# Kernel tuning notes

Hardware: AMD Instinct MI355X
Metric: run time of the kernel (lower is better)

Reference implementation:

```python
import jax, jax.numpy as jnp
import numpy as np

EPS = 1e-12  # torch F.normalize default eps

def _l2norm(x, axis=-1):
    n = jnp.linalg.norm(x, axis=axis, keepdims=True)
    return x / jnp.maximum(n, EPS)

def setup_inputs() -> dict:
    key = jax.random.key(0)
    k1, k2 = jax.random.split(key)
    query = jax.random.normal(k1, (65536, 512), dtype=jnp.float32)
    prototypes = jax.random.normal(k2, (64, 512), dtype=jnp.float32)
    return {"query": query, "prototypes": prototypes, "k": 3}

def reference(query, prototypes, k):
    # cosine similarity between queries and prototypes: [B, P]
    sim = jnp.einsum('bd,pd->bp', _l2norm(query), _l2norm(prototypes))
    k = min(int(k), prototypes.shape[0])
    weights, indices = jax.lax.top_k(sim, k)          # [B, k]
    retrieved = prototypes[indices]                   # [B, k, D]
    w = jax.nn.softmax(weights, axis=1)               # [B, k]
    return jnp.einsum('bkd,bk->bd', retrieved, w)     # [B, D]
```

## Files before the change

### kernel.cpp

```cpp
#include <hip/hip_runtime.h>
#include <math.h>

#define DIM   512
#define NP    64
#define TRB   128
#define BK    32
#define NCH   16
#define ASTR  132
#define TAU   1e-5f
#define RFB   128

#define WS_PTRAW 0
#define WS_INV64 131072
#define WS_INVPF 131584
#define WS_CNT   131840
#define WS_LIST  131968

__device__ __forceinline__ void ins4f(float v, int idx, float& v0, float& v1,
                                      float& v2, float& v3, int& j0, int& j1,
                                      int& j2, int& j3) {
  const bool b0 = v > v0, b1 = v > v1, b2 = v > v2, b3 = v > v3;
  v3 = b2 ? v2 : (b3 ? v : v3);  j3 = b2 ? j2 : (b3 ? idx : j3);
  v2 = b1 ? v1 : (b2 ? v : v2);  j2 = b1 ? j1 : (b2 ? idx : j2);
  v1 = b0 ? v0 : (b1 ? v : v1);  j1 = b0 ? j0 : (b1 ? idx : j1);
  v0 = b0 ? v  : v0;             j0 = b0 ? idx : j0;
}

__device__ __forceinline__ void ins3d(double v, int idx, double& b0, double& b1,
                                      double& b2, int& k0, int& k1, int& k2) {
  const bool c0 = v > b0, c1 = v > b1, c2 = v > b2;
  b2 = c1 ? b1 : (c2 ? v : b2);  k2 = c1 ? k1 : (c2 ? idx : k2);
  b1 = c0 ? b0 : (c1 ? v : b1);  k1 = c0 ? k0 : (c1 ? idx : k1);
  b0 = c0 ? v  : b0;             k0 = c0 ? idx : k0;
}

__global__ __launch_bounds__(256) void prep_kernel(
    const float* __restrict__ protos, float* __restrict__ ptw,
    double* __restrict__ inv64, float* __restrict__ invpf,
    int* __restrict__ cnt) {
  if (blockIdx.x == 0 && threadIdx.x == 0) *cnt = 0;
  const int p = (blockIdx.x * 256 + threadIdx.x) >> 6;
  const int lane = threadIdx.x & 63;
  if (p >= NP) return;
  const float4* pr = (const float4*)(protos + (size_t)p * DIM);
  const float4 a = pr[lane * 2];
  const float4 b = pr[lane * 2 + 1];
  double ss = (double)a.x * a.x + (double)a.y * a.y + (double)a.z * a.z +
              (double)a.w * a.w + (double)b.x * b.x + (double)b.y * b.y +
              (double)b.z * b.z + (double)b.w * b.w;
#pragma unroll
  for (int m = 1; m < 64; m <<= 1) ss += __shfl_xor(ss, m);
  const double inv = 1.0 / fmax(sqrt(ss), 1e-12);
  if (lane == 0) { inv64[p] = inv; invpf[p] = (float)inv; }
  const float v[8] = {a.x, a.y, a.z, a.w, b.x, b.y, b.z, b.w};
#pragma unroll
  for (int e = 0; e < 8; ++e)
    ptw[(size_t)(lane * 8 + e) * NP + p] = v[e];
}

__global__ __launch_bounds__(256, 4) void sim_kernel(
    const float* __restrict__ query, const float* __restrict__ protos,
    const float* __restrict__ ptw, const float* __restrict__ invpf,
    float* __restrict__ out, int* __restrict__ cnt, int* __restrict__ list) {
  __shared__ float Ast[BK * ASTR];
  __shared__ float Bst[BK * NP];
  __shared__ float nredL[TRB * 8];
  __shared__ float qiS[TRB];
  __shared__ float4 wiS[TRB];

  const int t = threadIdx.x;
  const int row0 = blockIdx.x * TRB;
  const int tr = t >> 4;
  const int tp = t & 15;
  const int arow = t >> 3;
  const int acp = t & 7;

  const float* aptr[4];
#pragma unroll
  for (int s = 0; s < 4; ++s)
    aptr[s] = query + (size_t)(row0 + arow + 32 * s) * DIM + acp * 4;
  const float* bptr = ptw + t * 8;

  float acc[8][4] = {};
  float na[4] = {0.f, 0.f, 0.f, 0.f};

  float4 Ar[4], Br0, Br1;
#pragma unroll
  for (int s = 0; s < 4; ++s) Ar[s] = *(const float4*)(aptr[s]);
  Br0 = *(const float4*)(bptr);
  Br1 = *(const float4*)(bptr + 4);

  for (int c = 0; c < NCH; ++c) {
    __syncthreads();
#pragma unroll
    for (int s = 0; s < 4; ++s) {
      const float v[4] = {Ar[s].x, Ar[s].y, Ar[s].z, Ar[s].w};
      const int rl = arow + 32 * s;
#pragma unroll
      for (int e = 0; e < 4; ++e) Ast[(acp * 4 + e) * ASTR + rl] = v[e];
      na[s] += v[0] * v[0] + v[1] * v[1] + v[2] * v[2] + v[3] * v[3];
    }
    *(float4*)&Bst[t * 8] = Br0;
    *(float4*)&Bst[t * 8 + 4] = Br1;
    __syncthreads();
    if (c + 1 < NCH) {
#pragma unroll
      for (int s = 0; s < 4; ++s)
        Ar[s] = *(const float4*)(aptr[s] + (c + 1) * BK);
      Br0 = *(const float4*)(bptr + (c + 1) * BK * NP);
      Br1 = *(const float4*)(bptr + (c + 1) * BK * NP + 4);
    }
#pragma unroll 8
    for (int kk = 0; kk < BK; ++kk) {
      const float4 a0 = *(const float4*)&Ast[kk * ASTR + tr * 8];
      const float4 a1 = *(const float4*)&Ast[kk * ASTR + tr * 8 + 4];
      const float4 b0 = *(const float4*)&Bst[kk * NP + tp * 4];
      const float av[8] = {a0.x, a0.y, a0.z, a0.w, a1.x, a1.y, a1.z, a1.w};
      const float bv[4] = {b0.x, b0.y, b0.z, b0.w};
#pragma unroll
      for (int i = 0; i < 8; ++i)
#pragma unroll
        for (int j = 0; j < 4; ++j)
          acc[i][j] = fmaf(av[i], bv[j], acc[i][j]);
    }
  }

#pragma unroll
  for (int s = 0; s < 4; ++s) nredL[(arow + 32 * s) * 8 + acp] = na[s];
  __syncthreads();
  if (t < TRB) {
    float ssum = 0.f;
#pragma unroll
    for (int e = 0; e < 8; ++e) ssum += nredL[t * 8 + e];
    qiS[t] = 1.0f / fmaxf(sqrtf(ssum), 1e-12f);
  }
  __syncthreads();

  const float4 ipv = *(const float4*)(invpf + tp * 4);
  const float ip[4] = {ipv.x, ipv.y, ipv.z, ipv.w};
#pragma unroll
  for (int i = 0; i < 8; ++i) {
    const int row = tr * 8 + i;
    float v0 = -1e30f, v1 = -1e30f, v2 = -1e30f, v3 = -1e30f;
    int j0 = 0, j1 = 0, j2 = 0, j3 = 0;
#pragma unroll
    for (int j = 0; j < 4; ++j)
      ins4f(acc[i][j] * ip[j], tp * 4 + j, v0, v1, v2, v3, j0, j1, j2, j3);
#pragma unroll
    for (int m = 1; m <= 8; m <<= 1) {
      const float p0 = __shfl_xor(v0, m), p1 = __shfl_xor(v1, m);
      const float p2 = __shfl_xor(v2, m), p3 = __shfl_xor(v3, m);
      const int q0 = __shfl_xor(j0, m), q1 = __shfl_xor(j1, m);
      const int q2 = __shfl_xor(j2, m), q3 = __shfl_xor(j3, m);
      ins4f(p0, q0, v0, v1, v2, v3, j0, j1, j2, j3);
      ins4f(p1, q1, v0, v1, v2, v3, j0, j1, j2, j3);
      ins4f(p2, q2, v0, v1, v2, v3, j0, j1, j2, j3);
      ins4f(p3, q3, v0, v1, v2, v3, j0, j1, j2, j3);
    }
    if (tp == 0) {
      const float qi = qiS[row];
      const float s0 = v0 * qi, s1 = v1 * qi, s2 = v2 * qi, s3 = v3 * qi;
      const float e1 = expf(s1 - s0), e2 = expf(s2 - s0);
      const float inv = 1.0f / (1.0f + e1 + e2);
      wiS[row] = make_float4(inv, e1 * inv, e2 * inv,
                             __int_as_float(j0 | (j1 << 6) | (j2 << 12)));
      if (s2 - s3 < TAU) {
        const int pos = atomicAdd(cnt, 1);
        list[pos] = row0 + row;
      }
    }
  }
  __syncthreads();

  const int wid = t >> 6;
  const int lane = t & 63;
#pragma unroll 4
  for (int it = 0; it < 64; ++it) {
    const int idx = it * 4 + wid;
    const int r = idx >> 1, h = idx & 1;
    const float4 wi = wiS[r];
    const int pack = __float_as_int(wi.w);
    const int i0 = pack & 63, i1 = (pack >> 6) & 63, i2 = (pack >> 12) & 63;
    const float4 pa = ((const float4*)(protos + (size_t)i0 * DIM + h * 256))[lane];
    const float4 pb = ((const float4*)(protos + (size_t)i1 * DIM + h * 256))[lane];
    const float4 pc = ((const float4*)(protos + (size_t)i2 * DIM + h * 256))[lane];
    float4 res;
    res.x = wi.x * pa.x + wi.y * pb.x + wi.z * pc.x;
    res.y = wi.x * pa.y + wi.y * pb.y + wi.z * pc.y;
    res.z = wi.x * pa.z + wi.y * pb.z + wi.z * pc.z;
    res.w = wi.x * pa.w + wi.y * pb.w + wi.z * pc.w;
    ((float4*)(out + (size_t)(row0 + r) * DIM + h * 256))[lane] = res;
  }
}

__global__ __launch_bounds__(256) void refine_kernel(
    const float* __restrict__ query, const float* __restrict__ protos,
    const float* __restrict__ ptw, const double* __restrict__ inv64,
    const int* __restrict__ cnt, const int* __restrict__ list,
    float* __restrict__ out) {
  const int n = *cnt;
  const int lane = threadIdx.x & 63;
  const int gw = blockIdx.x * 4 + (threadIdx.x >> 6);

  for (int i = gw; i < n; i += RFB * 4) {
    const int row = list[i];
    const float* q = query + (size_t)row * DIM;
    double a0 = 0.0, a1 = 0.0, a2 = 0.0, a3 = 0.0;
    float qs = 0.f;
#pragma unroll 4
    for (int k = 0; k < DIM; k += 4) {
      const float4 qv = *(const float4*)(q + k);
      a0 = fma((double)qv.x, (double)ptw[(size_t)(k + 0) * NP + lane], a0);
      a1 = fma((double)qv.y, (double)ptw[(size_t)(k + 1) * NP + lane], a1);
      a2 = fma((double)qv.z, (double)ptw[(size_t)(k + 2) * NP + lane], a2);
      a3 = fma((double)qv.w, (double)ptw[(size_t)(k + 3) * NP + lane], a3);
      qs += qv.x * qv.x + qv.y * qv.y + qv.z * qv.z + qv.w * qv.w;
    }
    const double sim = (a0 + a1 + a2 + a3) * inv64[lane];

    double b0 = sim, b1 = -1e300, b2 = -1e300;
    int k0 = lane, k1 = 0, k2 = 0;
#pragma unroll
    for (int m = 1; m <= 32; m <<= 1) {
      const double p0 = __shfl_xor(b0, m), p1 = __shfl_xor(b1, m),
                   p2 = __shfl_xor(b2, m);
      const int q0 = __shfl_xor(k0, m), q1 = __shfl_xor(k1, m),
                q2 = __shfl_xor(k2, m);
      ins3d(p0, q0, b0, b1, b2, k0, k1, k2);
      ins3d(p1, q1, b0, b1, b2, k0, k1, k2);
      ins3d(p2, q2, b0, b1, b2, k0, k1, k2);
    }
    const double qi = 1.0 / fmax(sqrt((double)qs), 1e-12);
    const double s0 = b0 * qi, s1 = b1 * qi, s2 = b2 * qi;
    const double e1 = exp(s1 - s0), e2 = exp(s2 - s0);
    const double inv = 1.0 / (1.0 + e1 + e2);
    const double w0 = inv, w1 = e1 * inv, w2 = e2 * inv;
    const float* p0r = protos + (size_t)k0 * DIM;
    const float* p1r = protos + (size_t)k1 * DIM;
    const float* p2r = protos + (size_t)k2 * DIM;
#pragma unroll
    for (int u = 0; u < 2; ++u) {
      const int col = u * 256 + lane * 4;
      const float4 x = *(const float4*)(p0r + col);
      const float4 y = *(const float4*)(p1r + col);
      const float4 z = *(const float4*)(p2r + col);
      float4 res;
      res.x = (float)(w0 * x.x + w1 * y.x + w2 * z.x);
      res.y = (float)(w0 * x.y + w1 * y.y + w2 * z.y);
      res.z = (float)(w0 * x.z + w1 * y.z + w2 * z.z);
      res.w = (float)(w0 * x.w + w1 * y.w + w2 * z.w);
      *(float4*)(out + (size_t)row * DIM + col) = res;
    }
  }
}

extern "C" void kernel_launch(void* const* d_in, const int* in_sizes, int n_in,
                              void* d_out, int out_size, void* d_ws, size_t ws_size,
                              hipStream_t stream) {
  const float* query = (const float*)d_in[0];
  const float* protos = (const float*)d_in[1];
  float* out = (float*)d_out;
  float* ptw = (float*)((char*)d_ws + WS_PTRAW);
  double* inv64 = (double*)((char*)d_ws + WS_INV64);
  float* invpf = (float*)((char*)d_ws + WS_INVPF);
  int* cnt = (int*)((char*)d_ws + WS_CNT);
  int* list = (int*)((char*)d_ws + WS_LIST);

  const int nrows = in_sizes[0] / DIM;

  hipLaunchKernelGGL(prep_kernel, dim3(16), dim3(256), 0, stream,
                     protos, ptw, inv64, invpf, cnt);
  hipLaunchKernelGGL(sim_kernel, dim3(nrows / TRB), dim3(256), 0, stream,
                     query, protos, ptw, invpf, out, cnt, list);
  hipLaunchKernelGGL(refine_kernel, dim3(RFB), dim3(256), 0, stream,
                     query, protos, ptw, inv64, cnt, list, out);
}
```

Before: 133.1 us.

## Halve row tile, double-buffer shared tiles with XOR swizzle, shuffle-reduce norms

```diff
diff --git a/kernel.cpp b/kernel.cpp
--- a/kernel.cpp
+++ b/kernel.cpp
@@ -3,10 +3,9 @@
 
 #define DIM   512
 #define NP    64
-#define TRB   128
+#define TRB   64
 #define BK    32
 #define NCH   16
-#define ASTR  132
 #define TAU   1e-5f
 #define RFB   128
 
@@ -62,9 +61,8 @@
     const float* __restrict__ query, const float* __restrict__ protos,
     const float* __restrict__ ptw, const float* __restrict__ invpf,
     float* __restrict__ out, int* __restrict__ cnt, int* __restrict__ list) {
-  __shared__ float Ast[BK * ASTR];
-  __shared__ float Bst[BK * NP];
-  __shared__ float nredL[TRB * 8];
+  __shared__ float Ast[2][BK][64];
+  __shared__ float Bst[2][BK][NP];
   __shared__ float qiS[TRB];
   __shared__ float4 wiS[TRB];
 
@@ -72,75 +70,77 @@
   const int row0 = blockIdx.x * TRB;
   const int tr = t >> 4;
   const int tp = t & 15;
-  const int arow = t >> 3;
-  const int acp = t & 7;
-
-  const float* aptr[4];
-#pragma unroll
-  for (int s = 0; s < 4; ++s)
-    aptr[s] = query + (size_t)(row0 + arow + 32 * s) * DIM + acp * 4;
-  const float* bptr = ptw + t * 8;
-
-  float acc[8][4] = {};
-  float na[4] = {0.f, 0.f, 0.f, 0.f};
-
-  float4 Ar[4], Br0, Br1;
-#pragma unroll
-  for (int s = 0; s < 4; ++s) Ar[s] = *(const float4*)(aptr[s]);
-  Br0 = *(const float4*)(bptr);
-  Br1 = *(const float4*)(bptr + 4);
-
-  for (int c = 0; c < NCH; ++c) {
+  const int sr = t >> 3;
+  const int sc = t & 7;
+  const int bk = t >> 4;
+  const int bp = t & 15;
+
+  const float* aptr0 = query + (size_t)(row0 + sr) * DIM + sc * 4;
+  const float* aptr1 = query + (size_t)(row0 + sr + 32) * DIM + sc * 4;
+  const float* bptr0 = ptw + (size_t)bk * NP + bp * 4;
+  const float* bptr1 = ptw + (size_t)(bk + 16) * NP + bp * 4;
+
+  float acc[4][4] = {};
+  float na0 = 0.f, na1 = 0.f;
+
+  float4 ar0 = *(const float4*)aptr0;
+  float4 ar1 = *(const float4*)aptr1;
+  float4 br0 = *(const float4*)bptr0;
+  float4 br1 = *(const float4*)bptr1;
+
+  const int rsw0 = sr ^ (sc << 2);
+  const int rsw1 = (sr + 32) ^ (sc << 2);
+
+  for (int ch = 0; ch < NCH; ++ch) {
+    const int b = ch & 1;
+    Ast[b][sc * 4 + 0][rsw0] = ar0.x;
+    Ast[b][sc * 4 + 1][rsw0] = ar0.y;
+    Ast[b][sc * 4 + 2][rsw0] = ar0.z;
+    Ast[b][sc * 4 + 3][rsw0] = ar0.w;
+    Ast[b][sc * 4 + 0][rsw1] = ar1.x;
+    Ast[b][sc * 4 + 1][rsw1] = ar1.y;
+    Ast[b][sc * 4 + 2][rsw1] = ar1.z;
+    Ast[b][sc * 4 + 3][rsw1] = ar1.w;
+    *(float4*)&Bst[b][bk][bp * 4] = br0;
+    *(float4*)&Bst[b][bk + 16][bp * 4] = br1;
+    na0 += ar0.x * ar0.x + ar0.y * ar0.y + ar0.z * ar0.z + ar0.w * ar0.w;
+    na1 += ar1.x * ar1.x + ar1.y * ar1.y + ar1.z * ar1.z + ar1.w * ar1.w;
     __syncthreads();
-#pragma unroll
-    for (int s = 0; s < 4; ++s) {
-      const float v[4] = {Ar[s].x, Ar[s].y, Ar[s].z, Ar[s].w};
-      const int rl = arow + 32 * s;
-#pragma unroll
-      for (int e = 0; e < 4; ++e) Ast[(acp * 4 + e) * ASTR + rl] = v[e];
-      na[s] += v[0] * v[0] + v[1] * v[1] + v[2] * v[2] + v[3] * v[3];
-    }
-    *(float4*)&Bst[t * 8] = Br0;
-    *(float4*)&Bst[t * 8 + 4] = Br1;
-    __syncthreads();
-    if (c + 1 < NCH) {
-#pragma unroll
-      for (int s = 0; s < 4; ++s)
-        Ar[s] = *(const float4*)(aptr[s] + (c + 1) * BK);
-      Br0 = *(const float4*)(bptr + (c + 1) * BK * NP);
-      Br1 = *(const float4*)(bptr + (c + 1) * BK * NP + 4);
+    if (ch + 1 < NCH) {
+      ar0 = *(const float4*)(aptr0 + (ch + 1) * BK);
+      ar1 = *(const float4*)(aptr1 + (ch + 1) * BK);
+      br0 = *(const float4*)(bptr0 + (size_t)(ch + 1) * BK * NP);
+      br1 = *(const float4*)(bptr1 + (size_t)(ch + 1) * BK * NP);
     }
 #pragma unroll 8
     for (int kk = 0; kk < BK; ++kk) {
-      const float4 a0 = *(const float4*)&Ast[kk * ASTR + tr * 8];
-      const float4 a1 = *(const float4*)&Ast[kk * ASTR + tr * 8 + 4];
-      const float4 b0 = *(const float4*)&Bst[kk * NP + tp * 4];
-      const float av[8] = {a0.x, a0.y, a0.z, a0.w, a1.x, a1.y, a1.z, a1.w};
-      const float bv[4] = {b0.x, b0.y, b0.z, b0.w};
-#pragma unroll
-      for (int i = 0; i < 8; ++i)
+      const int swz = (kk >> 2) << 2;
+      const float4 a4 = *(const float4*)&Ast[b][kk][(tr * 4) ^ swz];
+      const float4 b4 = *(const float4*)&Bst[b][kk][tp * 4];
+      const float av[4] = {a4.x, a4.y, a4.z, a4.w};
+      const float bv[4] = {b4.x, b4.y, b4.z, b4.w};
+#pragma unroll
+      for (int i = 0; i < 4; ++i)
 #pragma unroll
         for (int j = 0; j < 4; ++j)
           acc[i][j] = fmaf(av[i], bv[j], acc[i][j]);
     }
   }
 
-#pragma unroll
-  for (int s = 0; s < 4; ++s) nredL[(arow + 32 * s) * 8 + acp] = na[s];
-  __syncthreads();
-  if (t < TRB) {
-    float ssum = 0.f;
-#pragma unroll
-    for (int e = 0; e < 8; ++e) ssum += nredL[t * 8 + e];
-    qiS[t] = 1.0f / fmaxf(sqrtf(ssum), 1e-12f);
+  na0 += __shfl_xor(na0, 1); na1 += __shfl_xor(na1, 1);
+  na0 += __shfl_xor(na0, 2); na1 += __shfl_xor(na1, 2);
+  na0 += __shfl_xor(na0, 4); na1 += __shfl_xor(na1, 4);
+  if ((t & 7) == 0) {
+    qiS[sr] = 1.0f / fmaxf(sqrtf(na0), 1e-12f);
+    qiS[sr + 32] = 1.0f / fmaxf(sqrtf(na1), 1e-12f);
   }
   __syncthreads();
 
   const float4 ipv = *(const float4*)(invpf + tp * 4);
   const float ip[4] = {ipv.x, ipv.y, ipv.z, ipv.w};
 #pragma unroll
-  for (int i = 0; i < 8; ++i) {
-    const int row = tr * 8 + i;
+  for (int i = 0; i < 4; ++i) {
+    const int row = tr * 4 + i;
     float v0 = -1e30f, v1 = -1e30f, v2 = -1e30f, v3 = -1e30f;
     int j0 = 0, j1 = 0, j2 = 0, j3 = 0;
 #pragma unroll
@@ -175,7 +175,7 @@
   const int wid = t >> 6;
   const int lane = t & 63;
 #pragma unroll 4
-  for (int it = 0; it < 64; ++it) {
+  for (int it = 0; it < 32; ++it) {
     const int idx = it * 4 + wid;
     const int r = idx >> 1, h = idx & 1;
     const float4 wi = wiS[r];
```

Result: slower. 136.0 us (+2.2%).

## Restructure sim kernel to single-wavefront blocks with double-buffered 8x8 register tiles

Applied to the files above, without the earlier changes.

```diff
diff --git a/kernel.cpp b/kernel.cpp
--- a/kernel.cpp
+++ b/kernel.cpp
@@ -1,20 +1,17 @@
 #include <hip/hip_runtime.h>
 #include <math.h>
 
-#define DIM   512
-#define NP    64
-#define TRB   128
-#define BK    32
-#define NCH   16
-#define ASTR  132
-#define TAU   1e-5f
-#define RFB   128
+#define DIM 512
+#define NP  64
+#define TAU 1e-5f
+#define LISTCAP 8192
+#define RFB 128
 
 #define WS_PTRAW 0
-#define WS_INV64 131072
-#define WS_INVPF 131584
-#define WS_CNT   131840
-#define WS_LIST  131968
+#define WS_PTN   131072
+#define WS_INV64 262144
+#define WS_CNT   262656
+#define WS_LIST  262784
 
 __device__ __forceinline__ void ins4f(float v, int idx, float& v0, float& v1,
                                       float& v2, float& v3, int& j0, int& j1,
@@ -36,7 +33,7 @@
 
 __global__ __launch_bounds__(256) void prep_kernel(
     const float* __restrict__ protos, float* __restrict__ ptw,
-    double* __restrict__ inv64, float* __restrict__ invpf,
+    float* __restrict__ ptn, double* __restrict__ inv64,
     int* __restrict__ cnt) {
   if (blockIdx.x == 0 && threadIdx.x == 0) *cnt = 0;
   const int p = (blockIdx.x * 256 + threadIdx.x) >> 6;
@@ -51,103 +48,109 @@
 #pragma unroll
   for (int m = 1; m < 64; m <<= 1) ss += __shfl_xor(ss, m);
   const double inv = 1.0 / fmax(sqrt(ss), 1e-12);
-  if (lane == 0) { inv64[p] = inv; invpf[p] = (float)inv; }
+  if (lane == 0) inv64[p] = inv;
   const float v[8] = {a.x, a.y, a.z, a.w, b.x, b.y, b.z, b.w};
 #pragma unroll
-  for (int e = 0; e < 8; ++e)
-    ptw[(size_t)(lane * 8 + e) * NP + p] = v[e];
-}
-
-__global__ __launch_bounds__(256, 4) void sim_kernel(
+  for (int e = 0; e < 8; ++e) {
+    const size_t o = (size_t)(lane * 8 + e) * NP + p;
+    ptw[o] = v[e];
+    ptn[o] = (float)((double)v[e] * inv);
+  }
+}
+
+__global__ __launch_bounds__(64, 1) void sim_kernel(
     const float* __restrict__ query, const float* __restrict__ protos,
-    const float* __restrict__ ptw, const float* __restrict__ invpf,
-    float* __restrict__ out, int* __restrict__ cnt, int* __restrict__ list) {
-  __shared__ float Ast[BK * ASTR];
-  __shared__ float Bst[BK * NP];
-  __shared__ float nredL[TRB * 8];
-  __shared__ float qiS[TRB];
-  __shared__ float4 wiS[TRB];
-
-  const int t = threadIdx.x;
-  const int row0 = blockIdx.x * TRB;
-  const int tr = t >> 4;
-  const int tp = t & 15;
-  const int arow = t >> 3;
-  const int acp = t & 7;
-
-  const float* aptr[4];
-#pragma unroll
-  for (int s = 0; s < 4; ++s)
-    aptr[s] = query + (size_t)(row0 + arow + 32 * s) * DIM + acp * 4;
-  const float* bptr = ptw + t * 8;
-
-  float acc[8][4] = {};
-  float na[4] = {0.f, 0.f, 0.f, 0.f};
-
-  float4 Ar[4], Br0, Br1;
-#pragma unroll
-  for (int s = 0; s < 4; ++s) Ar[s] = *(const float4*)(aptr[s]);
-  Br0 = *(const float4*)(bptr);
-  Br1 = *(const float4*)(bptr + 4);
-
-  for (int c = 0; c < NCH; ++c) {
-    __syncthreads();
-#pragma unroll
-    for (int s = 0; s < 4; ++s) {
-      const float v[4] = {Ar[s].x, Ar[s].y, Ar[s].z, Ar[s].w};
-      const int rl = arow + 32 * s;
-#pragma unroll
-      for (int e = 0; e < 4; ++e) Ast[(acp * 4 + e) * ASTR + rl] = v[e];
-      na[s] += v[0] * v[0] + v[1] * v[1] + v[2] * v[2] + v[3] * v[3];
-    }
-    *(float4*)&Bst[t * 8] = Br0;
-    *(float4*)&Bst[t * 8 + 4] = Br1;
-    __syncthreads();
-    if (c + 1 < NCH) {
-#pragma unroll
-      for (int s = 0; s < 4; ++s)
-        Ar[s] = *(const float4*)(aptr[s] + (c + 1) * BK);
-      Br0 = *(const float4*)(bptr + (c + 1) * BK * NP);
-      Br1 = *(const float4*)(bptr + (c + 1) * BK * NP + 4);
-    }
+    const float* __restrict__ ptn, float* __restrict__ out,
+    int* __restrict__ cnt, int* __restrict__ list) {
+  __shared__ float Ast[2][32][64];
+  __shared__ float Bst[2][32][64];
+  __shared__ float qiS[64];
+  __shared__ float4 wiS[64];
+
+  const int l = threadIdx.x;
+  const int pg = l & 7;
+  const int rg = l >> 3;
+  const int row0 = blockIdx.x * 64;
+
+  const float* aq = query + (size_t)(row0 + l) * DIM;
+  const float* bq = ptn + l * 4;
+  const int bkw = l >> 4;
+  const int bpw = (l & 15) * 4;
+
+  float acc[8][8] = {};
+  float ss = 0.f;
+
+  {
+    float4 ar[8], br[8];
+#pragma unroll
+    for (int s = 0; s < 8; ++s) ar[s] = *(const float4*)(aq + s * 4);
+#pragma unroll
+    for (int s = 0; s < 8; ++s) br[s] = *(const float4*)(bq + s * 256);
+#pragma unroll
+    for (int s = 0; s < 8; ++s) {
+      Ast[0][s * 4 + 0][l] = ar[s].x;
+      Ast[0][s * 4 + 1][l] = ar[s].y;
+      Ast[0][s * 4 + 2][l] = ar[s].z;
+      Ast[0][s * 4 + 3][l] = ar[s].w;
+      *(float4*)&Bst[0][s * 4 + bkw][bpw] = br[s];
+      ss += ar[s].x * ar[s].x + ar[s].y * ar[s].y + ar[s].z * ar[s].z +
+            ar[s].w * ar[s].w;
+    }
+  }
+
+  for (int c = 0; c < 16; ++c) {
+    const int buf = c & 1;
+    float4 an[8], bn[8];
+    if (c < 15) {
+#pragma unroll
+      for (int s = 0; s < 8; ++s)
+        an[s] = *(const float4*)(aq + (c + 1) * 32 + s * 4);
+#pragma unroll
+      for (int s = 0; s < 8; ++s)
+        bn[s] = *(const float4*)(bq + (size_t)(c + 1) * 2048 + s * 256);
+    }
+    const float* Ab = &Ast[buf][0][rg * 8];
+    const float* Bb = &Bst[buf][0][pg * 8];
 #pragma unroll 8
-    for (int kk = 0; kk < BK; ++kk) {
-      const float4 a0 = *(const float4*)&Ast[kk * ASTR + tr * 8];
-      const float4 a1 = *(const float4*)&Ast[kk * ASTR + tr * 8 + 4];
-      const float4 b0 = *(const float4*)&Bst[kk * NP + tp * 4];
-      const float av[8] = {a0.x, a0.y, a0.z, a0.w, a1.x, a1.y, a1.z, a1.w};
-      const float bv[4] = {b0.x, b0.y, b0.z, b0.w};
+    for (int kk = 0; kk < 32; ++kk) {
+      const float4 A0 = *(const float4*)(Ab + kk * 64);
+      const float4 A1 = *(const float4*)(Ab + kk * 64 + 4);
+      const float4 B0 = *(const float4*)(Bb + kk * 64);
+      const float4 B1 = *(const float4*)(Bb + kk * 64 + 4);
+      const float av[8] = {A0.x, A0.y, A0.z, A0.w, A1.x, A1.y, A1.z, A1.w};
+      const float bv[8] = {B0.x, B0.y, B0.z, B0.w, B1.x, B1.y, B1.z, B1.w};
 #pragma unroll
       for (int i = 0; i < 8; ++i)
 #pragma unroll
-        for (int j = 0; j < 4; ++j)
+        for (int j = 0; j < 8; ++j)
           acc[i][j] = fmaf(av[i], bv[j], acc[i][j]);
     }
-  }
-
-#pragma unroll
-  for (int s = 0; s < 4; ++s) nredL[(arow + 32 * s) * 8 + acp] = na[s];
-  __syncthreads();
-  if (t < TRB) {
-    float ssum = 0.f;
-#pragma unroll
-    for (int e = 0; e < 8; ++e) ssum += nredL[t * 8 + e];
-    qiS[t] = 1.0f / fmaxf(sqrtf(ssum), 1e-12f);
-  }
-  __syncthreads();
-
-  const float4 ipv = *(const float4*)(invpf + tp * 4);
-  const float ip[4] = {ipv.x, ipv.y, ipv.z, ipv.w};
+    if (c < 15) {
+      const int nb = buf ^ 1;
+#pragma unroll
+      for (int s = 0; s < 8; ++s) {
+        Ast[nb][s * 4 + 0][l] = an[s].x;
+        Ast[nb][s * 4 + 1][l] = an[s].y;
+        Ast[nb][s * 4 + 2][l] = an[s].z;
+        Ast[nb][s * 4 + 3][l] = an[s].w;
+        *(float4*)&Bst[nb][s * 4 + bkw][bpw] = bn[s];
+        ss += an[s].x * an[s].x + an[s].y * an[s].y + an[s].z * an[s].z +
+              an[s].w * an[s].w;
+      }
+    }
+  }
+
+  qiS[l] = 1.0f / fmaxf(sqrtf(ss), 1e-12f);
+
 #pragma unroll
   for (int i = 0; i < 8; ++i) {
-    const int row = tr * 8 + i;
     float v0 = -1e30f, v1 = -1e30f, v2 = -1e30f, v3 = -1e30f;
     int j0 = 0, j1 = 0, j2 = 0, j3 = 0;
 #pragma unroll
-    for (int j = 0; j < 4; ++j)
-      ins4f(acc[i][j] * ip[j], tp * 4 + j, v0, v1, v2, v3, j0, j1, j2, j3);
-#pragma unroll
-    for (int m = 1; m <= 8; m <<= 1) {
+    for (int j = 0; j < 8; ++j)
+      ins4f(acc[i][j], pg * 8 + j, v0, v1, v2, v3, j0, j1, j2, j3);
+#pragma unroll
+    for (int m = 1; m <= 4; m <<= 1) {
       const float p0 = __shfl_xor(v0, m), p1 = __shfl_xor(v1, m);
       const float p2 = __shfl_xor(v2, m), p3 = __shfl_xor(v3, m);
       const int q0 = __shfl_xor(j0, m), q1 = __shfl_xor(j1, m);
@@ -157,7 +160,8 @@
       ins4f(p2, q2, v0, v1, v2, v3, j0, j1, j2, j3);
       ins4f(p3, q3, v0, v1, v2, v3, j0, j1, j2, j3);
     }
-    if (tp == 0) {
+    if (pg == 0) {
+      const int row = rg * 8 + i;
       const float qi = qiS[row];
       const float s0 = v0 * qi, s1 = v1 * qi, s2 = v2 * qi, s3 = v3 * qi;
       const float e1 = expf(s1 - s0), e2 = expf(s2 - s0);
@@ -166,30 +170,33 @@
                              __int_as_float(j0 | (j1 << 6) | (j2 << 12)));
       if (s2 - s3 < TAU) {
         const int pos = atomicAdd(cnt, 1);
-        list[pos] = row0 + row;
+        if (pos < LISTCAP) list[pos] = row0 + row;
       }
     }
   }
-  __syncthreads();
-
-  const int wid = t >> 6;
-  const int lane = t & 63;
-#pragma unroll 4
-  for (int it = 0; it < 64; ++it) {
-    const int idx = it * 4 + wid;
-    const int r = idx >> 1, h = idx & 1;
+
+#pragma unroll 2
+  for (int r = 0; r < 64; ++r) {
     const float4 wi = wiS[r];
     const int pack = __float_as_int(wi.w);
     const int i0 = pack & 63, i1 = (pack >> 6) & 63, i2 = (pack >> 12) & 63;
-    const float4 pa = ((const float4*)(protos + (size_t)i0 * DIM + h * 256))[lane];
-    const float4 pb = ((const float4*)(protos + (size_t)i1 * DIM + h * 256))[lane];
-    const float4 pc = ((const float4*)(protos + (size_t)i2 * DIM + h * 256))[lane];
-    float4 res;
-    res.x = wi.x * pa.x + wi.y * pb.x + wi.z * pc.x;
-    res.y = wi.x * pa.y + wi.y * pb.y + wi.z * pc.y;
-    res.z = wi.x * pa.z + wi.y * pb.z + wi.z * pc.z;
-    res.w = wi.x * pa.w + wi.y * pb.w + wi.z * pc.w;
-    ((float4*)(out + (size_t)(row0 + r) * DIM + h * 256))[lane] = res;
+    const float* p0 = protos + (size_t)i0 * DIM;
+    const float* p1 = protos + (size_t)i1 * DIM;
+    const float* p2 = protos + (size_t)i2 * DIM;
+    float* orow = out + (size_t)(row0 + r) * DIM;
+#pragma unroll
+    for (int h = 0; h < 2; ++h) {
+      const int col = h * 256 + l * 4;
+      const float4 x = *(const float4*)(p0 + col);
+      const float4 y = *(const float4*)(p1 + col);
+      const float4 z = *(const float4*)(p2 + col);
+      float4 res;
+      res.x = wi.x * x.x + wi.y * y.x + wi.z * z.x;
+      res.y = wi.x * x.y + wi.y * y.y + wi.z * z.y;
+      res.z = wi.x * x.z + wi.y * y.z + wi.z * z.z;
+      res.w = wi.x * x.w + wi.y * y.w + wi.z * z.w;
+      *(float4*)(orow + col) = res;
+    }
   }
 }
 
@@ -198,7 +205,7 @@
     const float* __restrict__ ptw, const double* __restrict__ inv64,
     const int* __restrict__ cnt, const int* __restrict__ list,
     float* __restrict__ out) {
-  const int n = *cnt;
+  const int n = min(*cnt, LISTCAP);
   const int lane = threadIdx.x & 63;
   const int gw = blockIdx.x * 4 + (threadIdx.x >> 6);
 
@@ -261,17 +268,17 @@
   const float* protos = (const float*)d_in[1];
   float* out = (float*)d_out;
   float* ptw = (float*)((char*)d_ws + WS_PTRAW);
+  float* ptn = (float*)((char*)d_ws + WS_PTN);
   double* inv64 = (double*)((char*)d_ws + WS_INV64);
-  float* invpf = (float*)((char*)d_ws + WS_INVPF);
   int* cnt = (int*)((char*)d_ws + WS_CNT);
   int* list = (int*)((char*)d_ws + WS_LIST);
 
   const int nrows = in_sizes[0] / DIM;
 
   hipLaunchKernelGGL(prep_kernel, dim3(16), dim3(256), 0, stream,
-                     protos, ptw, inv64, invpf, cnt);
-  hipLaunchKernelGGL(sim_kernel, dim3(nrows / TRB), dim3(256), 0, stream,
-                     query, protos, ptw, invpf, out, cnt, list);
+                     protos, ptw, ptn, inv64, cnt);
+  hipLaunchKernelGGL(sim_kernel, dim3(nrows / 64), dim3(64), 0, stream,
+                     query, protos, ptn, out, cnt, list);
   hipLaunchKernelGGL(refine_kernel, dim3(RFB), dim3(256), 0, stream,
                      query, protos, ptw, inv64, cnt, list, out);
 }
```

New measurement: 164.3 us. 1.23x slower.
